# Kernel tuning notes

Measured on AMD Instinct MI355X. Metric: run time of the kernel, lower is better.

Reference implementation:

```python
import jax, jax.numpy as jnp
import numpy as np

IN_CH, OUT_CH, K, POOL = 3, 16, 3, 2

def setup_inputs() -> dict:
    key = jax.random.key(0)
    kx, kw, kb = jax.random.split(key, 3)
    B, H, W = 64, 512, 512
    x = jax.random.normal(kx, (B, IN_CH, H, W), dtype=jnp.float32)
    fan_in = IN_CH * K * K
    bound = 1.0 / np.sqrt(fan_in)
    weight = jax.random.uniform(kw, (OUT_CH, IN_CH, K, K), dtype=jnp.float32, minval=-bound, maxval=bound)
    bias = jax.random.uniform(kb, (OUT_CH,), dtype=jnp.float32, minval=-bound, maxval=bound)
    return {"x": x, "weight": weight, "bias": bias}

def reference(x, weight, bias):
    # Conv2d, stride 1, VALID padding (matches in_h - k + 1 in kernel)
    y = jax.lax.conv_general_dilated(
        x, weight, window_strides=(1, 1), padding="VALID",
        dimension_numbers=("NCHW", "OIHW", "NCHW"))
    y = y + bias[None, :, None, None]  # [B, OC, Hc, Wc]
    B, C, Hc, Wc = y.shape
    Hp, Wp = Hc // POOL, Wc // POOL
    # Average pool 2x2 (floor-cropped like the CUDA kernel's integer division)
    y = y[:, :, :Hp * POOL, :Wp * POOL].reshape(B, C, Hp, POOL, Wp, POOL).mean(axis=(3, 5))
    # Sigmoid then sum over channel + spatial dims -> one scalar per batch element
    return jax.nn.sigmoid(y).sum(axis=(1, 2, 3))
```

## Files before the change

### kernel.cpp

```cpp
#include <hip/hip_runtime.h>


#define IC 3
#define OCH 16
#define HH 512
#define WW 512
#define WP 255
#define L 5
#define STRIPS 51

typedef float v2f __attribute__((ext_vector_type(2)));

__device__ __forceinline__ float fast_sigmoid(float v) {
    float e = __expf(-v);
    return __builtin_amdgcn_rcpf(1.0f + e);
}

__global__ void build_weff(const float* __restrict__ w,
                           const float* __restrict__ bias,
                           float* __restrict__ ws)
{
    const int i = threadIdx.x;
    for (int idx = i; idx < 384; idx += 256) {
        const int oc  = idx & 15;
        const int tap = idx >> 4;
        const int kx  = tap & 3;
        const int t2  = tap >> 2;
        const int kyp = t2 / 3;
        const int ic  = t2 - kyp * 3;
        float s[2];
#pragma unroll
        for (int which = 0; which < 2; ++which) {
            const int ky = which ? kyp : kyp + 2;
            float acc = 0.f;
#pragma unroll
            for (int py = 0; py < 2; ++py) {
                int r = ky - py;
                if (r < 0 || r > 2) continue;
#pragma unroll
                for (int px = 0; px < 2; ++px) {
                    int c = kx - px;
                    if (c < 0 || c > 2) continue;
                    acc += w[((oc * IC + ic) * 3 + r) * 3 + c];
                }
            }
            s[which] = 0.25f * acc;
        }
        ws[2 * idx]     = s[0];
        ws[2 * idx + 1] = s[1];
    }
    if (i < OCH) ws[768 + i] = bias[i];
}

#define LOADROW(buf, q)                                                  \
    {                                                                    \
        _Pragma("unroll")                                                \
        for (int ic_ = 0; ic_ < IC; ++ic_) {                             \
            const float* p_ = xb + (size_t)ic_ * (HH * WW)               \
                                 + (size_t)(q) * WW;                     \
            buf[ic_][0] = *(const v2f*)p_;                               \
            buf[ic_][1] = *(const v2f*)(p_ + 2);                         \
        }                                                                \
    }

#define TAPS(buf, kyp)                                                   \
    {                                                                    \
        _Pragma("unroll")                                                \
        for (int ic_ = 0; ic_ < IC; ++ic_) {                             \
            _Pragma("unroll")                                            \
            for (int kx_ = 0; kx_ < 4; ++kx_) {                          \
                const float xv_ = (kx_ < 2) ? buf[ic_][0][kx_]           \
                                            : buf[ic_][1][kx_ - 2];      \
                const v2f* wp_ = wtab + (((kyp) * IC + ic_) * 4 + kx_) * 16; \
                _Pragma("unroll")                                        \
                for (int oc_ = 0; oc_ < OCH; ++oc_)                      \
                    acc[oc_] += wp_[oc_] * xv_;                          \
            }                                                            \
        }                                                                \
    }

__global__ __launch_bounds__(256, 4)
void conv_pool_sig_sum(const float* __restrict__ x,
                       const float* __restrict__ ws,
                       float* __restrict__ out)
{
    const int tid = threadIdx.x;
    const int j = (tid < WP) ? tid : WP - 1;
    const int b = blockIdx.y;
    const int r0 = blockIdx.x * L;

    const v2f* __restrict__ wtab = (const v2f*)ws;
    const float* __restrict__ bs = ws + 768;

    const float* xb = x + (size_t)b * IC * HH * WW
                        + (size_t)(2 * r0) * WW + 2 * j;

    v2f xA[IC][2], xB[IC][2];
    LOADROW(xA, 0)
    LOADROW(xB, 1)

    v2f acc[OCH];
#pragma unroll
    for (int oc = 0; oc < OCH; ++oc) acc[oc] = (v2f){0.f, 0.f};

    float lsum = 0.f;

#pragma unroll 1
    for (int t = 0; t <= L; ++t) {
#pragma unroll
        for (int oc = 0; oc < OCH; ++oc) {
            acc[oc].x = acc[oc].y;
            acc[oc].y = bs[oc];
        }

        TAPS(xA, 0)
        { const int qa = (2 * t + 2 <= 2 * L + 1) ? (2 * t + 2) : (2 * L + 1);
          LOADROW(xA, qa) }

        TAPS(xB, 1)
        { const int qb = (2 * t + 3 <= 2 * L + 1) ? (2 * t + 3) : (2 * L + 1);
          LOADROW(xB, qb) }

        if (t > 0) {
#pragma unroll
            for (int oc = 0; oc < OCH; ++oc) lsum += fast_sigmoid(acc[oc].x);
        }
    }

    if (tid >= WP) lsum = 0.f;

#pragma unroll
    for (int off = 32; off > 0; off >>= 1)
        lsum += __shfl_xor(lsum, off, 64);
    if ((tid & 63) == 0) atomicAdd(out + b, lsum);
}

extern "C" void kernel_launch(void* const* d_in, const int* in_sizes, int n_in,
                              void* d_out, int out_size, void* d_ws, size_t ws_size,
                              hipStream_t stream) {
    const float* x = (const float*)d_in[0];
    const float* w = (const float*)d_in[1];
    const float* bias = (const float*)d_in[2];
    float* out = (float*)d_out;
    float* wws = (float*)d_ws;

    hipMemsetAsync(out, 0, out_size * sizeof(float), stream);
    build_weff<<<1, 256, 0, stream>>>(w, bias, wws);

    dim3 grid(STRIPS, 64);
    conv_pool_sig_sum<<<grid, 256, 0, stream>>>(x, wws, out);
}
```

Before: 405.1 us.

## Split output channels across threads with per-thread register weights

Restructures the work split so each thread handles one output channel for one pooled column, instead of one column across all 16 channels. Weights are held in registers per thread rather than read from a shared global table. The grid becomes 3D (column blocks × batch × row strips) with longer strips, and each block does one atomic after a shared-memory reduction. Each input value is now loaded by 16 threads, which raises load traffic that the cache has to absorb, and the sigmoid count per thread drops.

```diff
diff --git a/kernel.cpp b/kernel.cpp
--- a/kernel.cpp
+++ b/kernel.cpp
@@ -6,10 +6,13 @@
 #define HH 512
 #define WW 512
 #define WP 255
-#define L 5
-#define STRIPS 51
+#define L 15
+#define STRIPS 17
+#define CB 16
+#define NCB 16
 
 typedef float v2f __attribute__((ext_vector_type(2)));
+typedef float v4f __attribute__((ext_vector_type(4)));
 
 __device__ __forceinline__ float fast_sigmoid(float v) {
     float e = __expf(-v);
@@ -21,47 +24,35 @@
                            float* __restrict__ ws)
 {
     const int i = threadIdx.x;
-    for (int idx = i; idx < 384; idx += 256) {
-        const int oc  = idx & 15;
-        const int tap = idx >> 4;
-        const int kx  = tap & 3;
-        const int t2  = tap >> 2;
+    for (int idx = i; idx < OCH * 48; idx += 256) {
+        const int oc = idx / 48;
+        const int r  = idx - oc * 48;
+        const int tp = r >> 1;
+        const int which = r & 1;
+        const int kx = tp & 3;
+        const int t2 = tp >> 2;
         const int kyp = t2 / 3;
         const int ic  = t2 - kyp * 3;
-        float s[2];
+        const int ky = which ? kyp : (kyp + 2);
+        float s = 0.f;
 #pragma unroll
-        for (int which = 0; which < 2; ++which) {
-            const int ky = which ? kyp : kyp + 2;
-            float acc = 0.f;
+        for (int py = 0; py < 2; ++py) {
+            int rr = ky - py;
+            if (rr < 0 || rr > 2) continue;
 #pragma unroll
-            for (int py = 0; py < 2; ++py) {
-                int r = ky - py;
-                if (r < 0 || r > 2) continue;
-#pragma unroll
-                for (int px = 0; px < 2; ++px) {
-                    int c = kx - px;
-                    if (c < 0 || c > 2) continue;
-                    acc += w[((oc * IC + ic) * 3 + r) * 3 + c];
-                }
+            for (int px = 0; px < 2; ++px) {
+                int cc = kx - px;
+                if (cc < 0 || cc > 2) continue;
+                s += w[((oc * IC + ic) * 3 + rr) * 3 + cc];
             }
-            s[which] = 0.25f * acc;
         }
-        ws[2 * idx]     = s[0];
-        ws[2 * idx + 1] = s[1];
+        ws[oc * 64 + r] = 0.25f * s;
     }
-    if (i < OCH) ws[768 + i] = bias[i];
+    if (i < OCH) ws[i * 64 + 48] = bias[i];
 }
 
-#define LOADROW(buf, q)                                                  \
-    {                                                                    \
-        _Pragma("unroll")                                                \
-        for (int ic_ = 0; ic_ < IC; ++ic_) {                             \
-            const float* p_ = xb + (size_t)ic_ * (HH * WW)               \
-                                 + (size_t)(q) * WW;                     \
-            buf[ic_][0] = *(const v2f*)p_;                               \
-            buf[ic_][1] = *(const v2f*)(p_ + 2);                         \
-        }                                                                \
-    }
+#define WPAIR(P) (((P) & 1) ? (v2f){w4[(P) >> 1].z, w4[(P) >> 1].w} \
+                            : (v2f){w4[(P) >> 1].x, w4[(P) >> 1].y})
 
 #define TAPS(buf, kyp)                                                   \
     {                                                                    \
@@ -71,13 +62,26 @@
             for (int kx_ = 0; kx_ < 4; ++kx_) {                          \
                 const float xv_ = (kx_ < 2) ? buf[ic_][0][kx_]           \
                                             : buf[ic_][1][kx_ - 2];      \
-                const v2f* wp_ = wtab + (((kyp) * IC + ic_) * 4 + kx_) * 16; \
-                _Pragma("unroll")                                        \
-                for (int oc_ = 0; oc_ < OCH; ++oc_)                      \
-                    acc[oc_] += wp_[oc_] * xv_;                          \
+                const v2f wp_ = WPAIR(((kyp) * 3 + ic_) * 4 + kx_);      \
+                if (((ic_ * 4 + kx_) & 1) == 0) acc0 += wp_ * xv_;       \
+                else                            acc1 += wp_ * xv_;       \
             }                                                            \
         }                                                                \
     }
+
+#define PREFETCH(ebuf, obuf, offe, offo)                                 \
+    {                                                                    \
+        _Pragma("unroll")                                                \
+        for (int ic_ = 0; ic_ < IC; ++ic_) {                             \
+            const float* p_ = xr + (size_t)ic_ * (HH * WW);              \
+            ebuf[ic_][0] = *(const v2f*)(p_ + (offe));                   \
+            ebuf[ic_][1] = *(const v2f*)(p_ + (offe) + 2);               \
+            obuf[ic_][0] = *(const v2f*)(p_ + (offo));                   \
+            obuf[ic_][1] = *(const v2f*)(p_ + (offo) + 2);               \
+        }                                                                \
+    }
+
+#define ROTATE { acc0.x = acc0.y; acc0.y = bv;  acc1.x = acc1.y; acc1.y = 0.f; }
 
 __global__ __launch_bounds__(256, 4)
 void conv_pool_sig_sum(const float* __restrict__ x,
@@ -85,54 +89,65 @@
                        float* __restrict__ out)
 {
     const int tid = threadIdx.x;
-    const int j = (tid < WP) ? tid : WP - 1;
-    const int b = blockIdx.y;
-    const int r0 = blockIdx.x * L;
+    const int oc  = tid & 15;
+    const int jj  = blockIdx.x * CB + (tid >> 4);
+    const int j   = (jj < WP) ? jj : (WP - 1);
+    const int b   = blockIdx.y;
+    const int r0  = blockIdx.z * L;
 
-    const v2f* __restrict__ wtab = (const v2f*)ws;
-    const float* __restrict__ bs = ws + 768;
+    v4f w4[12];
+#pragma unroll
+    for (int k = 0; k < 12; ++k)
+        w4[k] = *(const v4f*)(ws + oc * 64 + 4 * k);
+    const float bv = ws[oc * 64 + 48];
 
-    const float* xb = x + (size_t)b * IC * HH * WW
+    const float* xr = x + (size_t)b * (IC * HH * WW)
                         + (size_t)(2 * r0) * WW + 2 * j;
 
-    v2f xA[IC][2], xB[IC][2];
-    LOADROW(xA, 0)
-    LOADROW(xB, 1)
+    v2f eA[IC][2], oA[IC][2], eB[IC][2], oB[IC][2];
 
-    v2f acc[OCH];
 #pragma unroll
-    for (int oc = 0; oc < OCH; ++oc) acc[oc] = (v2f){0.f, 0.f};
+    for (int ic = 0; ic < IC; ++ic) {
+        const float* p = xr + (size_t)ic * (HH * WW);
+        eA[ic][0] = *(const v2f*)(p);       eA[ic][1] = *(const v2f*)(p + 2);
+        oA[ic][0] = *(const v2f*)(p + WW);  oA[ic][1] = *(const v2f*)(p + WW + 2);
+    }
 
+    v2f acc0 = {0.f, 0.f}, acc1 = {0.f, 0.f};
     float lsum = 0.f;
 
 #pragma unroll 1
-    for (int t = 0; t <= L; ++t) {
-#pragma unroll
-        for (int oc = 0; oc < OCH; ++oc) {
-            acc[oc].x = acc[oc].y;
-            acc[oc].y = bs[oc];
+    for (int t = 0; t < L; t += 2) {
+        ROTATE
+        PREFETCH(eB, oB, 2 * WW, 3 * WW)
+        TAPS(eA, 0)
+        TAPS(oA, 1)
+        if (t > 0) lsum += fast_sigmoid(acc0.x + acc1.x);
+        xr += 2 * WW;
+
+        ROTATE
+        {
+            const int oe = (t < L - 1) ? 2 * WW : WW;
+            const int oo = (t < L - 1) ? 3 * WW : WW;
+            PREFETCH(eA, oA, oe, oo)
         }
-
-        TAPS(xA, 0)
-        { const int qa = (2 * t + 2 <= 2 * L + 1) ? (2 * t + 2) : (2 * L + 1);
-          LOADROW(xA, qa) }
-
-        TAPS(xB, 1)
-        { const int qb = (2 * t + 3 <= 2 * L + 1) ? (2 * t + 3) : (2 * L + 1);
-          LOADROW(xB, qb) }
-
-        if (t > 0) {
-#pragma unroll
-            for (int oc = 0; oc < OCH; ++oc) lsum += fast_sigmoid(acc[oc].x);
-        }
+        TAPS(eB, 0)
+        TAPS(oB, 1)
+        lsum += fast_sigmoid(acc0.x + acc1.x);
+        xr += 2 * WW;
     }
 
-    if (tid >= WP) lsum = 0.f;
+    if (jj >= WP) lsum = 0.f;
 
 #pragma unroll
     for (int off = 32; off > 0; off >>= 1)
         lsum += __shfl_xor(lsum, off, 64);
-    if ((tid & 63) == 0) atomicAdd(out + b, lsum);
+
+    __shared__ float red[4];
+    if ((tid & 63) == 0) red[tid >> 6] = lsum;
+    __syncthreads();
+    if (tid == 0)
+        atomicAdd(out + b, red[0] + red[1] + red[2] + red[3]);
 }
 
 extern "C" void kernel_launch(void* const* d_in, const int* in_sizes, int n_in,
@@ -147,6 +162,6 @@
     hipMemsetAsync(out, 0, out_size * sizeof(float), stream);
     build_weff<<<1, 256, 0, stream>>>(w, bias, wws);
 
-    dim3 grid(STRIPS, 64);
+    dim3 grid(NCB, 64, STRIPS);
     conv_pool_sig_sum<<<grid, 256, 0, stream>>>(x, wws, out);
 }
```

New measurement: 623.6 us. 53.9% more time.
